# Performance work log

Hardware: AMD Instinct MI355X
Metric: run time of the kernel (lower is better)

## Reference

```python
import jax, jax.numpy as jnp
import numpy as np

B, T, D, H = 4, 4096, 4096, 128  # head_size = embedding_size // num_heads = 4096 // 32

def setup_inputs() -> dict:
    key = jax.random.key(0)
    kx, kq, kk, kv = jax.random.split(key, 4)
    x = jax.random.normal(kx, (B, T, D), dtype=jnp.float32)
    # Dense kernels (no bias), init scale 0.01 as in the module
    Wq = jax.random.normal(kq, (D, H), dtype=jnp.float32) * 0.01
    Wk = jax.random.normal(kk, (D, H), dtype=jnp.float32) * 0.01
    Wv = jax.random.normal(kv, (D, H), dtype=jnp.float32) * 0.01
    return {"x": x, "Wq": Wq, "Wk": Wk, "Wv": Wv}

def reference(x, Wq, Wk, Wv):
    # Single-head projections: (B,T,D) @ (D,H) -> (B,T,H)
    Q = jnp.einsum('btd,dh->bth', x, Wq)
    K = jnp.einsum('btd,dh->bth', x, Wk)
    V = jnp.einsum('btd,dh->bth', x, Wv)
    scale = 1.0 / jnp.sqrt(jnp.asarray(H, dtype=Q.dtype))
    scores = jnp.einsum('bth,bsh->bts', Q, K) * scale  # (B,T,S) full score matrix
    weights = jax.nn.softmax(scores, axis=-1)
    # dropout rate = 0.0 (deterministic/eval) -> identity
    out = jnp.einsum('bts,bsh->bth', weights, V)  # (B,T,H)
    return out
```

## Files before the change

kernel.cpp:

```cpp
#include <hip/hip_runtime.h>


typedef __bf16 bf16_t;
typedef bf16_t bf16x8 __attribute__((ext_vector_type(8)));
typedef float f32x4 __attribute__((ext_vector_type(4)));
typedef float f32x8 __attribute__((ext_vector_type(8)));

#define MFMA16(A, B, C) __builtin_amdgcn_mfma_f32_16x16x32_bf16((A), (B), (C), 0, 0, 0)

__device__ __forceinline__ void async_cp16(const bf16_t* g, bf16_t* lds) {
  __builtin_amdgcn_global_load_lds(
      (__attribute__((address_space(1))) unsigned int*)g,
      (__attribute__((address_space(3))) unsigned int*)lds, 16, 0, 0);
}

__global__ void tr_w(const float* __restrict__ w0, const float* __restrict__ w1,
                     const float* __restrict__ w2, bf16_t* __restrict__ wt) {
  __shared__ float tile[32][33];
  const int z = blockIdx.z;
  const float* src = (z == 0) ? w0 : (z == 1) ? w1 : w2;
  bf16_t* dst = wt + (size_t)z * 128 * 4096;
  const int c0 = blockIdx.x * 32;
  const int r0 = blockIdx.y * 32;
  const int tx = threadIdx.x, ty = threadIdx.y;
#pragma unroll
  for (int j = 0; j < 4; ++j)
    tile[ty + 8 * j][tx] = src[(size_t)(r0 + ty + 8 * j) * 128 + c0 + tx];
  __syncthreads();
#pragma unroll
  for (int j = 0; j < 4; ++j)
    dst[(size_t)(c0 + ty + 8 * j) * 4096 + r0 + tx] = (bf16_t)tile[tx][ty + 8 * j];
}

__global__ void tr_v(const bf16_t* __restrict__ v, bf16_t* __restrict__ vt) {
  __shared__ bf16_t tile[32][33];
  const int b = blockIdx.z;
  const bf16_t* src = v + (size_t)b * 4096 * 128;
  bf16_t* dst = vt + (size_t)b * 128 * 4096;
  const int c0 = blockIdx.x * 32;
  const int r0 = blockIdx.y * 32;
  const int tx = threadIdx.x, ty = threadIdx.y;
#pragma unroll
  for (int j = 0; j < 4; ++j)
    tile[ty + 8 * j][tx] = src[(size_t)(r0 + ty + 8 * j) * 128 + c0 + tx];
  __syncthreads();
#pragma unroll
  for (int j = 0; j < 4; ++j)
    dst[(size_t)(c0 + ty + 8 * j) * 4096 + r0 + tx] = tile[tx][ty + 8 * j];
}

__launch_bounds__(256, 1)
__global__ void qkv_proj(const float* __restrict__ x, const bf16_t* __restrict__ wt,
                         bf16_t* __restrict__ q, bf16_t* __restrict__ k,
                         bf16_t* __restrict__ v) {
  __shared__ __align__(16) bf16_t sA[32 * 64];
  __shared__ __align__(16) bf16_t sB[384 * 64];
  const int tid = threadIdx.x;
  const int w = tid >> 6, lane = tid & 63, lq = lane & 15, quad = lane >> 4;
  const int m0 = blockIdx.x * 32;
  const int arow = tid >> 3, apc = tid & 7;
  const int alc = apc ^ (arow & 7);

  f32x4 acc[2][6];
#pragma unroll
  for (int i = 0; i < 2; ++i)
#pragma unroll
    for (int j = 0; j < 6; ++j) acc[i][j] = (f32x4){0.f, 0.f, 0.f, 0.f};

  for (int kt = 0; kt < 64; ++kt) {
    __syncthreads();
    const float4* xs = (const float4*)(x + (size_t)(m0 + arow) * 4096 + kt * 64 + alc * 8);
    float4 f0 = xs[0], f1 = xs[1];
    {
      const bf16_t* wb = wt + kt * 64;
#pragma unroll
      for (int r = 0; r < 12; ++r) {
        int cid = r * 256 + tid;
        int n = cid >> 3, pc = cid & 7;
        int lc = pc ^ (n & 7);
        async_cp16(wb + (size_t)n * 4096 + lc * 8, sB + (size_t)cid * 8);
      }
    }
    {
      f32x8 ff = {f0.x, f0.y, f0.z, f0.w, f1.x, f1.y, f1.z, f1.w};
      *(bf16x8*)(sA + arow * 64 + apc * 8) = __builtin_convertvector(ff, bf16x8);
    }
    __syncthreads();
#pragma unroll
    for (int ks = 0; ks < 2; ++ks) {
      bf16x8 af[2], bfr[6];
      const int cc = ks * 4 + quad;
#pragma unroll
      for (int mt = 0; mt < 2; ++mt) {
        int row = mt * 16 + lq;
        af[mt] = *(const bf16x8*)(sA + row * 64 + ((cc ^ (row & 7)) << 3));
      }
#pragma unroll
      for (int nt = 0; nt < 6; ++nt) {
        int n = w * 96 + nt * 16 + lq;
        bfr[nt] = *(const bf16x8*)(sB + n * 64 + ((cc ^ (n & 7)) << 3));
      }
#pragma unroll
      for (int mt = 0; mt < 2; ++mt)
#pragma unroll
        for (int nt = 0; nt < 6; ++nt) acc[mt][nt] = MFMA16(af[mt], bfr[nt], acc[mt][nt]);
    }
  }
#pragma unroll
  for (int mt = 0; mt < 2; ++mt) {
#pragma unroll
    for (int nt = 0; nt < 6; ++nt) {
      int n = w * 96 + nt * 16 + lq;
      bf16_t* dst;
      int nn;
      if (n < 128) { dst = q; nn = n; }
      else if (n < 256) { dst = k; nn = n - 128; }
      else { dst = v; nn = n - 256; }
#pragma unroll
      for (int r = 0; r < 4; ++r) {
        int m = m0 + mt * 16 + quad * 4 + r;
        dst[(size_t)m * 128 + nn] = (bf16_t)acc[mt][nt][r];
      }
    }
  }
}

__launch_bounds__(256, 1)
__global__ void flash(const bf16_t* __restrict__ q, const bf16_t* __restrict__ kk,
                      const bf16_t* __restrict__ vt, float* __restrict__ opart,
                      float* __restrict__ mlm, float* __restrict__ mll) {
  __shared__ __align__(16) bf16_t sK[64 * 128];
  __shared__ __align__(16) bf16_t sV[128 * 64];
  __shared__ __align__(16) bf16_t sP[64 * 72];
  const int tid = threadIdx.x;
  const int w = tid >> 6, lane = tid & 63, lq = lane & 15, quad = lane >> 4;
  const int b = blockIdx.x & 3;
  const int qt = (blockIdx.x >> 2) & 63;
  const int sp = blockIdx.x >> 8;
  const int qrow0 = qt * 64;

  bf16x8 qf[4];
  {
    const bf16_t* qp = q + ((size_t)b * 4096 + qrow0 + w * 16 + lq) * 128 + quad * 8;
#pragma unroll
    for (int ks = 0; ks < 4; ++ks) qf[ks] = *(const bf16x8*)(qp + ks * 32);
  }

  f32x4 accO[8];
#pragma unroll
  for (int i = 0; i < 8; ++i) accO[i] = (f32x4){0.f, 0.f, 0.f, 0.f};
  float mrow[4] = {-1e30f, -1e30f, -1e30f, -1e30f};
  float lrow[4] = {0.f, 0.f, 0.f, 0.f};

  const bf16_t* kbase = kk + (size_t)b * 4096 * 128;
  const bf16_t* vbase = vt + (size_t)b * 128 * 4096;
  const float SCL = 0.08838834764831845f * 1.4426950408889634f;

  for (int it = sp * 16; it < sp * 16 + 16; ++it) {
    __syncthreads();
    {
      const bf16_t* ksrc = kbase + (size_t)it * 64 * 128;
#pragma unroll
      for (int r = 0; r < 4; ++r) {
        int cid = r * 256 + tid;
        int row = cid >> 4, pc = cid & 15;
        int lc = pc ^ (row & 15);
        async_cp16(ksrc + row * 128 + lc * 8, sK + (size_t)cid * 8);
      }
      const bf16_t* vsrc = vbase + it * 64;
#pragma unroll
      for (int r = 0; r < 4; ++r) {
        int cid = r * 256 + tid;
        int h = cid >> 3, pc = cid & 7;
        int lc = pc ^ (h & 7);
        async_cp16(vsrc + (size_t)h * 4096 + lc * 8, sV + (size_t)cid * 8);
      }
    }
    __syncthreads();

    f32x4 accS[4];
#pragma unroll
    for (int nt = 0; nt < 4; ++nt) accS[nt] = (f32x4){0.f, 0.f, 0.f, 0.f};
#pragma unroll
    for (int ks = 0; ks < 4; ++ks) {
      const int cc = ks * 4 + quad;
#pragma unroll
      for (int nt = 0; nt < 4; ++nt) {
        int row = nt * 16 + lq;
        bf16x8 kf = *(const bf16x8*)(sK + row * 128 + ((cc ^ (row & 15)) << 3));
        accS[nt] = MFMA16(qf[ks], kf, accS[nt]);
      }
    }

#pragma unroll
    for (int nt = 0; nt < 4; ++nt) accS[nt] *= SCL;
    float mx[4];
#pragma unroll
    for (int r = 0; r < 4; ++r) {
      float t0 = fmaxf(fmaxf(accS[0][r], accS[1][r]), fmaxf(accS[2][r], accS[3][r]));
#pragma unroll
      for (int msk = 1; msk < 16; msk <<= 1) t0 = fmaxf(t0, __shfl_xor(t0, msk));
      mx[r] = t0;
    }
    float al[4];
#pragma unroll
    for (int r = 0; r < 4; ++r) {
      float mn = fmaxf(mrow[r], mx[r]);
      al[r] = exp2f(mrow[r] - mn);
      mrow[r] = mn;
    }
    float ps[4] = {0.f, 0.f, 0.f, 0.f};
#pragma unroll
    for (int nt = 0; nt < 4; ++nt)
#pragma unroll
      for (int r = 0; r < 4; ++r) {
        float p = exp2f(accS[nt][r] - mrow[r]);
        accS[nt][r] = p;
        ps[r] += p;
      }
#pragma unroll
    for (int r = 0; r < 4; ++r) {
      float s = ps[r];
#pragma unroll
      for (int msk = 1; msk < 16; msk <<= 1) s += __shfl_xor(s, msk);
      lrow[r] = lrow[r] * al[r] + s;
    }
#pragma unroll
    for (int ot = 0; ot < 8; ++ot) {
      accO[ot][0] *= al[0]; accO[ot][1] *= al[1];
      accO[ot][2] *= al[2]; accO[ot][3] *= al[3];
    }

#pragma unroll
    for (int nt = 0; nt < 4; ++nt) {
      int key = nt * 16 + lq;
#pragma unroll
      for (int r = 0; r < 4; ++r) {
        int prow = w * 16 + quad * 4 + r;
        sP[prow * 72 + key] = (bf16_t)accS[nt][r];
      }
    }
    __syncthreads();

#pragma unroll
    for (int ks2 = 0; ks2 < 2; ++ks2) {
      const int cc = ks2 * 4 + quad;
      bf16x8 pf = *(const bf16x8*)(sP + (w * 16 + lq) * 72 + cc * 8);
#pragma unroll
      for (int ot = 0; ot < 8; ++ot) {
        int h = ot * 16 + lq;
        bf16x8 vf = *(const bf16x8*)(sV + h * 64 + ((cc ^ (h & 7)) << 3));
        accO[ot] = MFMA16(pf, vf, accO[ot]);
      }
    }
  }

  float* op = opart + ((size_t)(sp * 4 + b) * 4096 + qrow0 + w * 16) * 128;
#pragma unroll
  for (int ot = 0; ot < 8; ++ot)
#pragma unroll
    for (int r = 0; r < 4; ++r)
      op[(size_t)(quad * 4 + r) * 128 + ot * 16 + lq] = accO[ot][r];
  if (lq == 0) {
#pragma unroll
    for (int r = 0; r < 4; ++r) {
      size_t idx = (size_t)(sp * 4 + b) * 4096 + qrow0 + w * 16 + quad * 4 + r;
      mlm[idx] = mrow[r];
      mll[idx] = lrow[r];
    }
  }
}

__global__ void merge(const float* __restrict__ opart, const float* __restrict__ mlm,
                      const float* __restrict__ mll, float* __restrict__ out) {
  const int idx = blockIdx.x * 256 + threadIdx.x;
  const int h = idx & 127;
  const int row = idx >> 7;
  float m[4], l[4];
#pragma unroll
  for (int s = 0; s < 4; ++s) {
    m[s] = mlm[s * 16384 + row];
    l[s] = mll[s * 16384 + row];
  }
  float M = fmaxf(fmaxf(m[0], m[1]), fmaxf(m[2], m[3]));
  float L = 0.f, acc = 0.f;
#pragma unroll
  for (int s = 0; s < 4; ++s) {
    float wgt = exp2f(m[s] - M);
    L += wgt * l[s];
    acc += wgt * opart[((size_t)s * 16384 + row) * 128 + h];
  }
  out[idx] = acc / L;
}

extern "C" void kernel_launch(void* const* d_in, const int* in_sizes, int n_in,
                              void* d_out, int out_size, void* d_ws, size_t ws_size,
                              hipStream_t stream) {
  (void)in_sizes; (void)n_in; (void)out_size; (void)ws_size;
  const float* x  = (const float*)d_in[0];
  const float* wq = (const float*)d_in[1];
  const float* wk = (const float*)d_in[2];
  const float* wv = (const float*)d_in[3];

  char* ws = (char*)d_ws;
  bf16_t* wt  = (bf16_t*)ws;                         ws += (size_t)384 * 4096 * 2;
  bf16_t* qb  = (bf16_t*)ws;                         ws += (size_t)16384 * 128 * 2;
  bf16_t* kb  = (bf16_t*)ws;                         ws += (size_t)16384 * 128 * 2;
  bf16_t* vb  = (bf16_t*)ws;                         ws += (size_t)16384 * 128 * 2;
  bf16_t* vtb = (bf16_t*)ws;                         ws += (size_t)16384 * 128 * 2;
  float*  opart = (float*)ws;                        ws += (size_t)4 * 16384 * 128 * 4;
  float*  mlm = (float*)ws;                          ws += (size_t)4 * 16384 * 4;
  float*  mll = (float*)ws;
  float*  ob  = (float*)d_out;

  dim3 tb(32, 8, 1);
  tr_w<<<dim3(4, 128, 3), tb, 0, stream>>>(wq, wk, wv, wt);
  qkv_proj<<<dim3(512), dim3(256), 0, stream>>>(x, wt, qb, kb, vb);
  tr_v<<<dim3(4, 128, 4), tb, 0, stream>>>(vb, vtb);
  flash<<<dim3(1024), dim3(256), 0, stream>>>(qb, kb, vtb, opart, mlm, mll);
  merge<<<dim3(8192), dim3(256), 0, stream>>>(opart, mlm, mll, ob);
}
```

Before: 531.4 us.

## Double-buffer LDS in projection and flash kernels, halve split-K, skip redundant rescales

The QKV projection now uses 512-thread blocks over 64-row tiles. It double-buffers the x and weight tiles in LDS, so the loads for step k+1 are issued while the MFMAs for step k run. The flash kernel also double-buffers K/V tiles, raises wave priority around its MFMA blocks, and rescales the output accumulator only when some row max actually grows. It also drops the barrier before the P·V product, since each wave reads only the P rows it wrote. The split over keys goes from 4 to 2 partitions, which halves the partial-output traffic and simplifies the merge, at the cost of fewer flash blocks (512) for parallelism.

```diff
diff --git a/kernel.cpp b/kernel.cpp
--- a/kernel.cpp
+++ b/kernel.cpp
@@ -49,17 +49,30 @@
     dst[(size_t)(c0 + ty + 8 * j) * 4096 + r0 + tx] = tile[tx][ty + 8 * j];
 }
 
-__launch_bounds__(256, 1)
+__device__ __forceinline__ void stage_b(const bf16_t* __restrict__ wt_k,
+                                        bf16_t* sBbuf, int tid) {
+#pragma unroll
+  for (int r = 0; r < 6; ++r) {
+    int cid = r * 512 + tid;
+    int n = cid >> 3, pc = cid & 7;
+    int lc = pc ^ (n & 7);
+    async_cp16(wt_k + (size_t)n * 4096 + lc * 8, sBbuf + (size_t)cid * 8);
+  }
+}
+
+__launch_bounds__(512, 2)
 __global__ void qkv_proj(const float* __restrict__ x, const bf16_t* __restrict__ wt,
                          bf16_t* __restrict__ q, bf16_t* __restrict__ k,
                          bf16_t* __restrict__ v) {
-  __shared__ __align__(16) bf16_t sA[32 * 64];
-  __shared__ __align__(16) bf16_t sB[384 * 64];
+  __shared__ __align__(16) bf16_t sA[2][64 * 64];
+  __shared__ __align__(16) bf16_t sB[2][384 * 64];
   const int tid = threadIdx.x;
   const int w = tid >> 6, lane = tid & 63, lq = lane & 15, quad = lane >> 4;
-  const int m0 = blockIdx.x * 32;
+  const int wr = w >> 2, wc = w & 3;
+  const int m0 = blockIdx.x * 64;
   const int arow = tid >> 3, apc = tid & 7;
   const int alc = apc ^ (arow & 7);
+  const float* xrow = x + (size_t)(m0 + arow) * 4096 + alc * 8;
 
   f32x4 acc[2][6];
 #pragma unroll
@@ -67,50 +80,54 @@
 #pragma unroll
     for (int j = 0; j < 6; ++j) acc[i][j] = (f32x4){0.f, 0.f, 0.f, 0.f};
 
+  {
+    float4 f0 = ((const float4*)xrow)[0];
+    float4 f1 = ((const float4*)xrow)[1];
+    stage_b(wt, sB[0], tid);
+    f32x8 ff = {f0.x, f0.y, f0.z, f0.w, f1.x, f1.y, f1.z, f1.w};
+    *(bf16x8*)(sA[0] + arow * 64 + apc * 8) = __builtin_convertvector(ff, bf16x8);
+  }
+  __syncthreads();
+
   for (int kt = 0; kt < 64; ++kt) {
-    __syncthreads();
-    const float4* xs = (const float4*)(x + (size_t)(m0 + arow) * 4096 + kt * 64 + alc * 8);
-    float4 f0 = xs[0], f1 = xs[1];
-    {
-      const bf16_t* wb = wt + kt * 64;
-#pragma unroll
-      for (int r = 0; r < 12; ++r) {
-        int cid = r * 256 + tid;
-        int n = cid >> 3, pc = cid & 7;
-        int lc = pc ^ (n & 7);
-        async_cp16(wb + (size_t)n * 4096 + lc * 8, sB + (size_t)cid * 8);
-      }
-    }
-    {
-      f32x8 ff = {f0.x, f0.y, f0.z, f0.w, f1.x, f1.y, f1.z, f1.w};
-      *(bf16x8*)(sA + arow * 64 + apc * 8) = __builtin_convertvector(ff, bf16x8);
-    }
-    __syncthreads();
+    const int buf = kt & 1;
+    float4 f0, f1;
+    if (kt < 63) {
+      const float* xp = xrow + (kt + 1) * 64;
+      f0 = ((const float4*)xp)[0];
+      f1 = ((const float4*)xp)[1];
+      stage_b(wt + (kt + 1) * 64, sB[buf ^ 1], tid);
+    }
 #pragma unroll
     for (int ks = 0; ks < 2; ++ks) {
       bf16x8 af[2], bfr[6];
       const int cc = ks * 4 + quad;
 #pragma unroll
       for (int mt = 0; mt < 2; ++mt) {
-        int row = mt * 16 + lq;
-        af[mt] = *(const bf16x8*)(sA + row * 64 + ((cc ^ (row & 7)) << 3));
+        int row = wr * 32 + mt * 16 + lq;
+        af[mt] = *(const bf16x8*)(sA[buf] + row * 64 + ((cc ^ (row & 7)) << 3));
       }
 #pragma unroll
       for (int nt = 0; nt < 6; ++nt) {
-        int n = w * 96 + nt * 16 + lq;
-        bfr[nt] = *(const bf16x8*)(sB + n * 64 + ((cc ^ (n & 7)) << 3));
+        int n = wc * 96 + nt * 16 + lq;
+        bfr[nt] = *(const bf16x8*)(sB[buf] + n * 64 + ((cc ^ (n & 7)) << 3));
       }
 #pragma unroll
       for (int mt = 0; mt < 2; ++mt)
 #pragma unroll
         for (int nt = 0; nt < 6; ++nt) acc[mt][nt] = MFMA16(af[mt], bfr[nt], acc[mt][nt]);
     }
+    if (kt < 63) {
+      f32x8 ff = {f0.x, f0.y, f0.z, f0.w, f1.x, f1.y, f1.z, f1.w};
+      *(bf16x8*)(sA[buf ^ 1] + arow * 64 + apc * 8) = __builtin_convertvector(ff, bf16x8);
+    }
+    __syncthreads();
   }
 #pragma unroll
   for (int mt = 0; mt < 2; ++mt) {
 #pragma unroll
     for (int nt = 0; nt < 6; ++nt) {
-      int n = w * 96 + nt * 16 + lq;
+      int n = wc * 96 + nt * 16 + lq;
       bf16_t* dst;
       int nn;
       if (n < 128) { dst = q; nn = n; }
@@ -118,19 +135,38 @@
       else { dst = v; nn = n - 256; }
 #pragma unroll
       for (int r = 0; r < 4; ++r) {
-        int m = m0 + mt * 16 + quad * 4 + r;
+        int m = m0 + wr * 32 + mt * 16 + quad * 4 + r;
         dst[(size_t)m * 128 + nn] = (bf16_t)acc[mt][nt][r];
       }
     }
   }
 }
 
-__launch_bounds__(256, 1)
+__device__ __forceinline__ void stage_kv(const bf16_t* __restrict__ ksrc,
+                                         const bf16_t* __restrict__ vsrc,
+                                         bf16_t* sKbuf, bf16_t* sVbuf, int tid) {
+#pragma unroll
+  for (int r = 0; r < 4; ++r) {
+    int cid = r * 256 + tid;
+    int row = cid >> 4, pc = cid & 15;
+    int lc = pc ^ (row & 15);
+    async_cp16(ksrc + row * 128 + lc * 8, sKbuf + (size_t)cid * 8);
+  }
+#pragma unroll
+  for (int r = 0; r < 4; ++r) {
+    int cid = r * 256 + tid;
+    int h = cid >> 3, pc = cid & 7;
+    int lc = pc ^ (h & 7);
+    async_cp16(vsrc + (size_t)h * 4096 + lc * 8, sVbuf + (size_t)cid * 8);
+  }
+}
+
+__launch_bounds__(256, 2)
 __global__ void flash(const bf16_t* __restrict__ q, const bf16_t* __restrict__ kk,
                       const bf16_t* __restrict__ vt, float* __restrict__ opart,
                       float* __restrict__ mlm, float* __restrict__ mll) {
-  __shared__ __align__(16) bf16_t sK[64 * 128];
-  __shared__ __align__(16) bf16_t sV[128 * 64];
+  __shared__ __align__(16) bf16_t sK[2][64 * 128];
+  __shared__ __align__(16) bf16_t sV[2][128 * 64];
   __shared__ __align__(16) bf16_t sP[64 * 72];
   const int tid = threadIdx.x;
   const int w = tid >> 6, lane = tid & 63, lq = lane & 15, quad = lane >> 4;
@@ -155,66 +191,64 @@
   const bf16_t* kbase = kk + (size_t)b * 4096 * 128;
   const bf16_t* vbase = vt + (size_t)b * 128 * 4096;
   const float SCL = 0.08838834764831845f * 1.4426950408889634f;
-
-  for (int it = sp * 16; it < sp * 16 + 16; ++it) {
-    __syncthreads();
-    {
-      const bf16_t* ksrc = kbase + (size_t)it * 64 * 128;
-#pragma unroll
-      for (int r = 0; r < 4; ++r) {
-        int cid = r * 256 + tid;
-        int row = cid >> 4, pc = cid & 15;
-        int lc = pc ^ (row & 15);
-        async_cp16(ksrc + row * 128 + lc * 8, sK + (size_t)cid * 8);
-      }
-      const bf16_t* vsrc = vbase + it * 64;
-#pragma unroll
-      for (int r = 0; r < 4; ++r) {
-        int cid = r * 256 + tid;
-        int h = cid >> 3, pc = cid & 7;
-        int lc = pc ^ (h & 7);
-        async_cp16(vsrc + (size_t)h * 4096 + lc * 8, sV + (size_t)cid * 8);
-      }
-    }
-    __syncthreads();
+  const int it0 = sp * 32;
+
+  stage_kv(kbase + (size_t)it0 * 64 * 128, vbase + it0 * 64, sK[0], sV[0], tid);
+  __syncthreads();
+
+  for (int i = 0; i < 32; ++i) {
+    const int buf = i & 1;
+    if (i < 31)
+      stage_kv(kbase + (size_t)(it0 + i + 1) * 64 * 128, vbase + (it0 + i + 1) * 64,
+               sK[buf ^ 1], sV[buf ^ 1], tid);
 
     f32x4 accS[4];
 #pragma unroll
     for (int nt = 0; nt < 4; ++nt) accS[nt] = (f32x4){0.f, 0.f, 0.f, 0.f};
+    __builtin_amdgcn_s_setprio(1);
 #pragma unroll
     for (int ks = 0; ks < 4; ++ks) {
       const int cc = ks * 4 + quad;
 #pragma unroll
       for (int nt = 0; nt < 4; ++nt) {
         int row = nt * 16 + lq;
-        bf16x8 kf = *(const bf16x8*)(sK + row * 128 + ((cc ^ (row & 15)) << 3));
+        bf16x8 kf = *(const bf16x8*)(sK[buf] + row * 128 + ((cc ^ (row & 15)) << 3));
         accS[nt] = MFMA16(qf[ks], kf, accS[nt]);
       }
     }
-
-#pragma unroll
-    for (int nt = 0; nt < 4; ++nt) accS[nt] *= SCL;
-    float mx[4];
+    __builtin_amdgcn_s_setprio(0);
+
+    float mxs[4];
 #pragma unroll
     for (int r = 0; r < 4; ++r) {
       float t0 = fmaxf(fmaxf(accS[0][r], accS[1][r]), fmaxf(accS[2][r], accS[3][r]));
 #pragma unroll
       for (int msk = 1; msk < 16; msk <<= 1) t0 = fmaxf(t0, __shfl_xor(t0, msk));
-      mx[r] = t0;
-    }
-    float al[4];
-#pragma unroll
-    for (int r = 0; r < 4; ++r) {
-      float mn = fmaxf(mrow[r], mx[r]);
-      al[r] = exp2f(mrow[r] - mn);
-      mrow[r] = mn;
+      mxs[r] = t0 * SCL;
+    }
+    bool grow = (mxs[0] > mrow[0]) || (mxs[1] > mrow[1]) ||
+                (mxs[2] > mrow[2]) || (mxs[3] > mrow[3]);
+    if (__any(grow)) {
+      float al[4];
+#pragma unroll
+      for (int r = 0; r < 4; ++r) {
+        float mn = fmaxf(mrow[r], mxs[r]);
+        al[r] = exp2f(mrow[r] - mn);
+        mrow[r] = mn;
+        lrow[r] *= al[r];
+      }
+#pragma unroll
+      for (int ot = 0; ot < 8; ++ot) {
+        accO[ot][0] *= al[0]; accO[ot][1] *= al[1];
+        accO[ot][2] *= al[2]; accO[ot][3] *= al[3];
+      }
     }
     float ps[4] = {0.f, 0.f, 0.f, 0.f};
 #pragma unroll
     for (int nt = 0; nt < 4; ++nt)
 #pragma unroll
       for (int r = 0; r < 4; ++r) {
-        float p = exp2f(accS[nt][r] - mrow[r]);
+        float p = exp2f(fmaf(accS[nt][r], SCL, -mrow[r]));
         accS[nt][r] = p;
         ps[r] += p;
       }
@@ -223,12 +257,7 @@
       float s = ps[r];
 #pragma unroll
       for (int msk = 1; msk < 16; msk <<= 1) s += __shfl_xor(s, msk);
-      lrow[r] = lrow[r] * al[r] + s;
-    }
-#pragma unroll
-    for (int ot = 0; ot < 8; ++ot) {
-      accO[ot][0] *= al[0]; accO[ot][1] *= al[1];
-      accO[ot][2] *= al[2]; accO[ot][3] *= al[3];
+      lrow[r] += s;
     }
 
 #pragma unroll
@@ -240,8 +269,8 @@
         sP[prow * 72 + key] = (bf16_t)accS[nt][r];
       }
     }
-    __syncthreads();
-
+
+    __builtin_amdgcn_s_setprio(1);
 #pragma unroll
     for (int ks2 = 0; ks2 < 2; ++ks2) {
       const int cc = ks2 * 4 + quad;
@@ -249,10 +278,12 @@
 #pragma unroll
       for (int ot = 0; ot < 8; ++ot) {
         int h = ot * 16 + lq;
-        bf16x8 vf = *(const bf16x8*)(sV + h * 64 + ((cc ^ (h & 7)) << 3));
+        bf16x8 vf = *(const bf16x8*)(sV[buf] + h * 64 + ((cc ^ (h & 7)) << 3));
         accO[ot] = MFMA16(pf, vf, accO[ot]);
       }
     }
+    __builtin_amdgcn_s_setprio(0);
+    __syncthreads();
   }
 
   float* op = opart + ((size_t)(sp * 4 + b) * 4096 + qrow0 + w * 16) * 128;
@@ -276,20 +307,13 @@
   const int idx = blockIdx.x * 256 + threadIdx.x;
   const int h = idx & 127;
   const int row = idx >> 7;
-  float m[4], l[4];
-#pragma unroll
-  for (int s = 0; s < 4; ++s) {
-    m[s] = mlm[s * 16384 + row];
-    l[s] = mll[s * 16384 + row];
-  }
-  float M = fmaxf(fmaxf(m[0], m[1]), fmaxf(m[2], m[3]));
-  float L = 0.f, acc = 0.f;
-#pragma unroll
-  for (int s = 0; s < 4; ++s) {
-    float wgt = exp2f(m[s] - M);
-    L += wgt * l[s];
-    acc += wgt * opart[((size_t)s * 16384 + row) * 128 + h];
-  }
+  float m0 = mlm[row], m1 = mlm[16384 + row];
+  float l0 = mll[row], l1 = mll[16384 + row];
+  float M = fmaxf(m0, m1);
+  float w0 = exp2f(m0 - M), w1 = exp2f(m1 - M);
+  float L = w0 * l0 + w1 * l1;
+  float acc = w0 * opart[(size_t)row * 128 + h] +
+              w1 * opart[((size_t)16384 + row) * 128 + h];
   out[idx] = acc / L;
 }
 
@@ -308,15 +332,15 @@
   bf16_t* kb  = (bf16_t*)ws;                         ws += (size_t)16384 * 128 * 2;
   bf16_t* vb  = (bf16_t*)ws;                         ws += (size_t)16384 * 128 * 2;
   bf16_t* vtb = (bf16_t*)ws;                         ws += (size_t)16384 * 128 * 2;
-  float*  opart = (float*)ws;                        ws += (size_t)4 * 16384 * 128 * 4;
-  float*  mlm = (float*)ws;                          ws += (size_t)4 * 16384 * 4;
+  float*  opart = (float*)ws;                        ws += (size_t)2 * 16384 * 128 * 4;
+  float*  mlm = (float*)ws;                          ws += (size_t)2 * 16384 * 4;
   float*  mll = (float*)ws;
   float*  ob  = (float*)d_out;
 
   dim3 tb(32, 8, 1);
   tr_w<<<dim3(4, 128, 3), tb, 0, stream>>>(wq, wk, wv, wt);
-  qkv_proj<<<dim3(512), dim3(256), 0, stream>>>(x, wt, qb, kb, vb);
+  qkv_proj<<<dim3(256), dim3(512), 0, stream>>>(x, wt, qb, kb, vb);
   tr_v<<<dim3(4, 128, 4), tb, 0, stream>>>(vb, vtb);
-  flash<<<dim3(1024), dim3(256), 0, stream>>>(qb, kb, vtb, opart, mlm, mll);
+  flash<<<dim3(512), dim3(256), 0, stream>>>(qb, kb, vtb, opart, mlm, mll);
   merge<<<dim3(8192), dim3(256), 0, stream>>>(opart, mlm, mll, ob);
 }
```

New measurement: 529.0 us. No clear change (-0.5%).
